# Performance work log

Measured on AMD Instinct MI355X. Metric: run time of the kernel, lower is better.

The kernel has to match this reference:

```python
import jax, jax.numpy as jnp
import numpy as np

N_NODES = 100000
N_EDGES = 1600000
FEATURE_DIM, CONDITION_DIM, HIDDEN_DIM, LATENT_DIM = 256, 64, 128, 64


def setup_inputs() -> dict:
    key = jax.random.key(0)
    ks = jax.random.split(key, 12)

    def glorot(k, fan_in, fan_out):
        s = np.sqrt(6.0 / (fan_in + fan_out)).astype(np.float32)
        return jax.random.uniform(k, (fan_in, fan_out), jnp.float32, -s, s)

    return {
        "feature": jax.random.normal(ks[0], (N_NODES, FEATURE_DIM), jnp.float32),
        "condition": jax.random.normal(ks[1], (N_NODES, CONDITION_DIM), jnp.float32),
        "edge_index": jax.random.randint(ks[2], (2, N_EDGES), 0, N_NODES, jnp.int64),
        "W_f2h": glorot(ks[3], FEATURE_DIM, HIDDEN_DIM),
        "b_f2h": jnp.zeros((HIDDEN_DIM,), jnp.float32),
        "W_c2h": glorot(ks[4], CONDITION_DIM, HIDDEN_DIM),
        "b_c2h": jnp.zeros((HIDDEN_DIM,), jnp.float32),
        "W_h2h": glorot(ks[5], 2 * HIDDEN_DIM, HIDDEN_DIM),
        "b_h2h": jnp.zeros((HIDDEN_DIM,), jnp.float32),
        "W_h2l": glorot(ks[6], HIDDEN_DIM, LATENT_DIM),
        "b_h2l": jnp.zeros((LATENT_DIM,), jnp.float32),
    }


def reference(feature, condition, edge_index, W_f2h, b_f2h, W_c2h, b_c2h,
              W_h2h, b_h2h, W_h2l, b_h2l):
    N = feature.shape[0]
    self_loops = jnp.arange(N, dtype=edge_index.dtype)
    src = jnp.concatenate([edge_index[0], self_loops])  # message sources (j)
    dst = jnp.concatenate([edge_index[1], self_loops])  # message targets (i)

    # symmetric GCN normalization: D^{-1/2} (A+I) D^{-1/2}
    deg = jax.ops.segment_sum(jnp.ones(dst.shape[0], feature.dtype), dst,
                              num_segments=N)
    dinv = jnp.where(deg > 0, jax.lax.rsqrt(deg), 0.0)
    norm = dinv[src] * dinv[dst]  # [E+N]

    def gcn_conv(x, W, b):
        xl = x @ W                                   # [N, out]
        msg = xl[src] * norm[:, None]                # gather + scale
        return jax.ops.segment_sum(msg, dst, num_segments=N) + b

    f2h = jnp.tanh(gcn_conv(feature, W_f2h, b_f2h))
    c2h = jnp.tanh(gcn_conv(condition, W_c2h, b_c2h))
    h = jnp.concatenate([f2h, c2h], axis=1)          # [N, 2*hidden]
    h = jnp.tanh(gcn_conv(h, W_h2h, b_h2h))
    z = gcn_conv(h, W_h2l, b_h2l)
    return z
```

## Files before the change

### kernel.cpp

```cpp
#include <hip/hip_runtime.h>
#include <cmath>
#include <cstdint>


typedef _Float16 f16;
typedef _Float16 f16x8 __attribute__((ext_vector_type(8)));
typedef _Float16 f16x4 __attribute__((ext_vector_type(4)));
typedef float f32x4 __attribute__((ext_vector_type(4)));
typedef unsigned int u32x4 __attribute__((ext_vector_type(4)));
typedef unsigned int u32x2 __attribute__((ext_vector_type(2)));

__global__ void count_zero_kernel(int* __restrict__ count, int N) {
    int i = blockIdx.x * 256 + threadIdx.x;
    if (i < N) count[i] = 0;
}

__global__ void count_rank_kernel(const int* __restrict__ dst, int* __restrict__ count,
                                  int* __restrict__ rank, int E) {
    int e = blockIdx.x * 256 + threadIdx.x;
    if (e < E) rank[e] = atomicAdd(&count[dst[e]], 1);
}

constexpr int SCAN_VPT = 8;
constexpr int SCAN_TILE = 256 * SCAN_VPT;

__global__ __launch_bounds__(256) void scan_partial_kernel(const int* __restrict__ count,
                                                           float* __restrict__ dinv,
                                                           int* __restrict__ blocksums, int N) {
    __shared__ int red[256];
    const int t = threadIdx.x;
    int base = blockIdx.x * SCAN_TILE + t * SCAN_VPT;
    int s = 0;
#pragma unroll
    for (int i = 0; i < SCAN_VPT; ++i) {
        int idx = base + i;
        if (idx < N) {
            int c = count[idx];
            dinv[idx] = rsqrtf((float)(c + 1));
            s += c;
        }
    }
    red[t] = s;
    __syncthreads();
    for (int off = 128; off > 0; off >>= 1) {
        if (t < off) red[t] += red[t + off];
        __syncthreads();
    }
    if (t == 0) blocksums[blockIdx.x] = red[0];
}

__global__ __launch_bounds__(256) void scan_final_kernel(const int* __restrict__ count,
                                                         const int* __restrict__ blocksums,
                                                         int* __restrict__ row_ptr, int N, int nb) {
    __shared__ int red[256];
    __shared__ int bs[64];
    const int t = threadIdx.x;
    if (t < 64) bs[t] = (t < nb) ? blocksums[t] : 0;
    __syncthreads();
    for (int off = 1; off < 64; off <<= 1) {
        int u = (t < 64 && t >= off) ? bs[t - off] : 0;
        __syncthreads();
        if (t < 64) bs[t] += u;
        __syncthreads();
    }
    const int myBase = (blockIdx.x > 0) ? bs[blockIdx.x - 1] : 0;

    int base = blockIdx.x * SCAN_TILE + t * SCAN_VPT;
    int vals[SCAN_VPT];
    int s = 0;
#pragma unroll
    for (int i = 0; i < SCAN_VPT; ++i) {
        int idx = base + i;
        vals[i] = (idx < N) ? count[idx] : 0;
        s += vals[i];
    }
    red[t] = s;
    __syncthreads();
    for (int off = 1; off < 256; off <<= 1) {
        int u = (t >= off) ? red[t - off] : 0;
        __syncthreads();
        red[t] += u;
        __syncthreads();
    }
    int run = red[t] - s + myBase;
#pragma unroll
    for (int i = 0; i < SCAN_VPT; ++i) {
        int idx = base + i;
        if (idx < N) {
            row_ptr[idx] = run;
            run += vals[i];
            if (idx == N - 1) row_ptr[N] = run;
        }
    }
}

__global__ void fill_kernel(const int* __restrict__ src, const int* __restrict__ dst,
                            const int* __restrict__ rank, const float* __restrict__ dinv,
                            const int* __restrict__ row_ptr, long long* __restrict__ csr, int E) {
    int e = blockIdx.x * 256 + threadIdx.x;
    if (e >= E) return;
    int s = src[e];
    int d = dst[e];
    int pos = row_ptr[d] + rank[e];
    float nrm = dinv[s] * dinv[d];
    long long v = ((long long)(unsigned)__float_as_int(nrm) << 32) | (unsigned)s;
    __builtin_nontemporal_store(v, csr + pos);
}

__device__ inline void wprep_one(const float* __restrict__ W, f16* __restrict__ hi,
                                 f16* __restrict__ lo, int M, int idx) {
    int k = idx / M, m = idx % M;
    float w = W[idx];
    f16 h = (f16)w;
    int f = ((k >> 5) * (M >> 4) + (m >> 4)) * 512 + (((k >> 3) & 3) << 7) + ((m & 15) << 3) + (k & 7);
    hi[f] = h;
    lo[f] = (f16)(w - (float)h);
}

__global__ void wprep_all_kernel(const float* __restrict__ W1, f16* h1, f16* l1,
                                 const float* __restrict__ W2, f16* h2, f16* l2,
                                 const float* __restrict__ W3, f16* h3, f16* l3,
                                 const float* __restrict__ W4, f16* h4, f16* l4) {
    int b = blockIdx.x;
    int t = threadIdx.x;
    if (b < 128) {
        wprep_one(W1, h1, l1, 128, b * 256 + t);
    } else if (b < 160) {
        wprep_one(W2, h2, l2, 128, (b - 128) * 256 + t);
    } else if (b < 288) {
        wprep_one(W3, h3, l3, 128, (b - 160) * 256 + t);
    } else {
        wprep_one(W4, h4, l4, 64, (b - 288) * 256 + t);
    }
}

__global__ void cond_to_xl_kernel(const float* __restrict__ x, f16* __restrict__ XL, int N) {
    int i = blockIdx.x * 256 + threadIdx.x;
    if (i >= N * 16) return;
    int node = i >> 4, q = i & 15;
    float4 v = ((const float4*)x)[i];
    union { f16 h[4]; uint2 u; } p;
    p.h[0] = (f16)v.x; p.h[1] = (f16)v.y; p.h[2] = (f16)v.z; p.h[3] = (f16)v.w;
    *(uint2*)(XL + (size_t)node * 192 + 128 + q * 4) = p.u;
}

template <int K, int M, bool BIAS_TANH, bool X_IS_HALF>
__global__ __launch_bounds__(256) void gemm_direct_kernel(
    const void* __restrict__ Xv, const f16* __restrict__ WFh,
    const f16* __restrict__ WFl, const float* __restrict__ bias,
    f16* __restrict__ out, int ld, int colOff, int ldx, int N) {
    constexpr int BM = 128;
    constexpr int SW = M / 4;
    constexpr int CT = SW / 16;
    constexpr int RT = BM / 16;
    constexpr int KS = K / 32;
    constexpr int MT = M / 16;

    const int tid = threadIdx.x;
    const int lane = tid & 63;
    const int wv = tid >> 6;
    const int m16 = lane & 15;
    const int quad = lane >> 4;
    const int row0 = blockIdx.x * BM;

    int xr[RT];
#pragma unroll
    for (int rt = 0; rt < RT; ++rt) {
        int r = row0 + rt * 16 + m16;
        xr[rt] = r < N ? r : N - 1;
    }

    f32x4 acc[RT][CT];
#pragma unroll
    for (int rt = 0; rt < RT; ++rt)
#pragma unroll
        for (int ct = 0; ct < CT; ++ct) acc[rt][ct] = (f32x4){0.f, 0.f, 0.f, 0.f};

    for (int ks = 0; ks < KS; ++ks) {
        const int k0 = ks * 32;
        f16x8 bh[CT], bl[CT];
#pragma unroll
        for (int ct = 0; ct < CT; ++ct) {
            const int fb = ((ks * MT + wv * CT + ct) << 9) + lane * 8;
            bh[ct] = *(const f16x8*)(WFh + fb);
            bl[ct] = *(const f16x8*)(WFl + fb);
        }
#pragma unroll
        for (int rt = 0; rt < RT; ++rt) {
            f16x8 a;
            if (X_IS_HALF) {
                a = *(const f16x8*)((const f16*)Xv + (size_t)xr[rt] * ldx + k0 + quad * 8);
            } else {
                const float* xp = (const float*)Xv + (size_t)xr[rt] * ldx + k0 + quad * 8;
                f32x4 v0 = *(const f32x4*)xp;
                f32x4 v1 = *(const f32x4*)(xp + 4);
                a[0] = (f16)v0[0]; a[1] = (f16)v0[1]; a[2] = (f16)v0[2]; a[3] = (f16)v0[3];
                a[4] = (f16)v1[0]; a[5] = (f16)v1[1]; a[6] = (f16)v1[2]; a[7] = (f16)v1[3];
            }
#pragma unroll
            for (int ct = 0; ct < CT; ++ct) {
                acc[rt][ct] = __builtin_amdgcn_mfma_f32_16x16x32_f16(a, bh[ct], acc[rt][ct], 0, 0, 0);
                acc[rt][ct] = __builtin_amdgcn_mfma_f32_16x16x32_f16(a, bl[ct], acc[rt][ct], 0, 0, 0);
            }
        }
    }

    float brs[CT];
    if (BIAS_TANH) {
#pragma unroll
        for (int ct = 0; ct < CT; ++ct) brs[ct] = bias[wv * SW + ct * 16 + m16];
    }

#pragma unroll
    for (int rt = 0; rt < RT; ++rt) {
#pragma unroll
        for (int r = 0; r < 4; ++r) {
            int row = row0 + rt * 16 + quad * 4 + r;
            if (row < N) {
                f16* op = out + (size_t)row * ld + colOff + wv * SW + m16;
#pragma unroll
                for (int ct = 0; ct < CT; ++ct) {
                    float v = acc[rt][ct][r];
                    if (BIAS_TANH) v = tanhf(v + brs[ct]);
                    op[ct * 16] = (f16)v;
                }
            }
        }
    }
}

template <int M, bool TANH, bool HAS_BIAS, bool OUT_F32>
__global__ __launch_bounds__(256) void gather_h_kernel(
    const f16* __restrict__ xl, const float* __restrict__ b,
    const float* __restrict__ dinv, const int* __restrict__ row_ptr,
    const long long* __restrict__ csr, void* __restrict__ outv,
    int ld, int colOff, int N) {
    constexpr int TPN = M / 8;
    int gid = blockIdx.x * 256 + threadIdx.x;
    int node = gid / TPN;
    int t = gid % TPN;
    if (node >= N) return;

    float di = dinv[node];
    float self = di * di;
    f16x8 x = *(const f16x8*)(xl + (size_t)node * M + t * 8);
    float acc[8];
#pragma unroll
    for (int j = 0; j < 8; ++j) acc[j] = (float)x[j] * self;
    if (HAS_BIAS) {
        float4 b0 = *(const float4*)(b + t * 8);
        float4 b1 = *(const float4*)(b + t * 8 + 4);
        acc[0] += b0.x; acc[1] += b0.y; acc[2] += b0.z; acc[3] += b0.w;
        acc[4] += b1.x; acc[5] += b1.y; acc[6] += b1.z; acc[7] += b1.w;
    }

    int p = row_ptr[node];
    const int p1 = row_ptr[node + 1];
    const int last = p1 - 1;
    long long e0 = 0, e1 = 0, e2 = 0, e3 = 0;
    if (p < p1) {
        e0 = __builtin_nontemporal_load(csr + p);
        e1 = __builtin_nontemporal_load(csr + (p + 1 < p1 ? p + 1 : last));
        e2 = __builtin_nontemporal_load(csr + (p + 2 < p1 ? p + 2 : last));
        e3 = __builtin_nontemporal_load(csr + (p + 3 < p1 ? p + 3 : last));
    }
    while (p < p1) {
        const long long c0 = e0, c1 = e1, c2 = e2, c3 = e3;
        const int pn = p + 4;
        if (pn < p1) {
            e0 = __builtin_nontemporal_load(csr + pn);
            e1 = __builtin_nontemporal_load(csr + (pn + 1 < p1 ? pn + 1 : last));
            e2 = __builtin_nontemporal_load(csr + (pn + 2 < p1 ? pn + 2 : last));
            e3 = __builtin_nontemporal_load(csr + (pn + 3 < p1 ? pn + 3 : last));
        }
        int s0 = (int)c0, s1 = (int)c1, s2 = (int)c2, s3 = (int)c3;
        float n0 = __int_as_float((int)(c0 >> 32));
        float n1 = (p + 1 < p1) ? __int_as_float((int)(c1 >> 32)) : 0.f;
        float n2 = (p + 2 < p1) ? __int_as_float((int)(c2 >> 32)) : 0.f;
        float n3 = (p + 3 < p1) ? __int_as_float((int)(c3 >> 32)) : 0.f;
        f16x8 v0 = *(const f16x8*)(xl + (size_t)s0 * M + t * 8);
        f16x8 v1 = *(const f16x8*)(xl + (size_t)s1 * M + t * 8);
        f16x8 v2 = *(const f16x8*)(xl + (size_t)s2 * M + t * 8);
        f16x8 v3 = *(const f16x8*)(xl + (size_t)s3 * M + t * 8);
#pragma unroll
        for (int j = 0; j < 8; ++j)
            acc[j] += ((float)v0[j] * n0 + (float)v1[j] * n1) +
                      ((float)v2[j] * n2 + (float)v3[j] * n3);
        p = pn;
    }

    if (TANH) {
#pragma unroll
        for (int j = 0; j < 8; ++j) acc[j] = tanhf(acc[j]);
    }

    if (OUT_F32) {
        float* op = (float*)outv + (size_t)node * ld + colOff + t * 8;
        f32x4 o0 = {acc[0], acc[1], acc[2], acc[3]};
        f32x4 o1 = {acc[4], acc[5], acc[6], acc[7]};
        __builtin_nontemporal_store(o0, (f32x4*)op);
        __builtin_nontemporal_store(o1, (f32x4*)(op + 4));
    } else {
        union { f16 h[8]; u32x4 u; } o;
#pragma unroll
        for (int j = 0; j < 8; ++j) o.h[j] = (f16)acc[j];
        __builtin_nontemporal_store(o.u, (u32x4*)((f16*)outv + (size_t)node * ld + colOff + t * 8));
    }
}

__global__ __launch_bounds__(256) void gather_fused_kernel(
    const f16* __restrict__ XL, const float* __restrict__ bA,
    const float* __restrict__ dinv, const int* __restrict__ row_ptr,
    const long long* __restrict__ csr, f16* __restrict__ out, int N) {
    int gid = blockIdx.x * 256 + threadIdx.x;
    int node = gid >> 4;
    int t = gid & 15;
    if (node >= N) return;

    float di = dinv[node];
    float self = di * di;
    const f16* base = XL + (size_t)node * 192;
    f16x8 xa = *(const f16x8*)(base + t * 8);
    f16x4 xc = *(const f16x4*)(base + 128 + t * 4);
    float accA[8], accC[4];
#pragma unroll
    for (int j = 0; j < 8; ++j) accA[j] = (float)xa[j] * self;
#pragma unroll
    for (int j = 0; j < 4; ++j) accC[j] = (float)xc[j] * self;
    {
        float4 b0 = *(const float4*)(bA + t * 8);
        float4 b1 = *(const float4*)(bA + t * 8 + 4);
        accA[0] += b0.x; accA[1] += b0.y; accA[2] += b0.z; accA[3] += b0.w;
        accA[4] += b1.x; accA[5] += b1.y; accA[6] += b1.z; accA[7] += b1.w;
    }

    int p = row_ptr[node];
    const int p1 = row_ptr[node + 1];
    const int last = p1 - 1;
    long long e0 = 0, e1 = 0, e2 = 0, e3 = 0;
    if (p < p1) {
        e0 = __builtin_nontemporal_load(csr + p);
        e1 = __builtin_nontemporal_load(csr + (p + 1 < p1 ? p + 1 : last));
        e2 = __builtin_nontemporal_load(csr + (p + 2 < p1 ? p + 2 : last));
        e3 = __builtin_nontemporal_load(csr + (p + 3 < p1 ? p + 3 : last));
    }
    while (p < p1) {
        const long long c0 = e0, c1 = e1, c2 = e2, c3 = e3;
        const int pn = p + 4;
        if (pn < p1) {
            e0 = __builtin_nontemporal_load(csr + pn);
            e1 = __builtin_nontemporal_load(csr + (pn + 1 < p1 ? pn + 1 : last));
            e2 = __builtin_nontemporal_load(csr + (pn + 2 < p1 ? pn + 2 : last));
            e3 = __builtin_nontemporal_load(csr + (pn + 3 < p1 ? pn + 3 : last));
        }
        int s0 = (int)c0, s1 = (int)c1, s2 = (int)c2, s3 = (int)c3;
        float n0 = __int_as_float((int)(c0 >> 32));
        float n1 = (p + 1 < p1) ? __int_as_float((int)(c1 >> 32)) : 0.f;
        float n2 = (p + 2 < p1) ? __int_as_float((int)(c2 >> 32)) : 0.f;
        float n3 = (p + 3 < p1) ? __int_as_float((int)(c3 >> 32)) : 0.f;
        const f16* r0 = XL + (size_t)s0 * 192;
        const f16* r1 = XL + (size_t)s1 * 192;
        const f16* r2 = XL + (size_t)s2 * 192;
        const f16* r3 = XL + (size_t)s3 * 192;
        f16x8 a0 = *(const f16x8*)(r0 + t * 8);
        f16x8 a1 = *(const f16x8*)(r1 + t * 8);
        f16x8 a2 = *(const f16x8*)(r2 + t * 8);
        f16x8 a3 = *(const f16x8*)(r3 + t * 8);
        f16x4 q0 = *(const f16x4*)(r0 + 128 + t * 4);
        f16x4 q1 = *(const f16x4*)(r1 + 128 + t * 4);
        f16x4 q2 = *(const f16x4*)(r2 + 128 + t * 4);
        f16x4 q3 = *(const f16x4*)(r3 + 128 + t * 4);
#pragma unroll
        for (int j = 0; j < 8; ++j)
            accA[j] += ((float)a0[j] * n0 + (float)a1[j] * n1) +
                       ((float)a2[j] * n2 + (float)a3[j] * n3);
#pragma unroll
        for (int j = 0; j < 4; ++j)
            accC[j] += ((float)q0[j] * n0 + (float)q1[j] * n1) +
                       ((float)q2[j] * n2 + (float)q3[j] * n3);
        p = pn;
    }

#pragma unroll
    for (int j = 0; j < 8; ++j) accA[j] = tanhf(accA[j]);

    union { f16 h[8]; u32x4 u; } oa;
#pragma unroll
    for (int j = 0; j < 8; ++j) oa.h[j] = (f16)accA[j];
    __builtin_nontemporal_store(oa.u, (u32x4*)(out + (size_t)node * 256 + t * 8));
    union { f16 h[4]; u32x2 u; } oc;
#pragma unroll
    for (int j = 0; j < 4; ++j) oc.h[j] = (f16)accC[j];
    __builtin_nontemporal_store(oc.u, (u32x2*)(out + (size_t)node * 256 + 128 + t * 4));
}

extern "C" void kernel_launch(void* const* d_in, const int* in_sizes, int n_in,
                              void* d_out, int out_size, void* d_ws, size_t ws_size,
                              hipStream_t stream) {
    const int FD = 256;

    const float* feature   = (const float*)d_in[0];
    const float* condition = (const float*)d_in[1];
    const int*   edge      = (const int*)d_in[2];
    const float* W_f2h = (const float*)d_in[3];
    const float* b_f2h = (const float*)d_in[4];
    const float* W_c2h = (const float*)d_in[5];
    const float* b_c2h = (const float*)d_in[6];
    const float* W_h2h = (const float*)d_in[7];
    const float* b_h2h = (const float*)d_in[8];
    const float* W_h2l = (const float*)d_in[9];
    const float* b_h2l = (const float*)d_in[10];
    float* out = (float*)d_out;

    const int N = in_sizes[0] / FD;
    const int E = in_sizes[2] / 2;
    const int* src = edge;
    const int* dst = edge + E;

    float* ws_f   = (float*)d_ws;
    float* dinv   = ws_f;
    int*   count  = (int*)(ws_f + N);
    int*   rowp   = count + N;
    int*   bsums  = rowp + N + 1;
    int*   rank   = bsums + 1024;
    long long* csr = (long long*)(((uintptr_t)(rank + E) + 15) & ~(uintptr_t)15);
    f16*   XL     = (f16*)(csr + E);
    f16*   B_h    = XL + (size_t)N * 192;
    f16*   wt1h   = B_h + (size_t)N * 256;
    f16*   wt1l   = wt1h + 128 * 256;
    f16*   wt2h   = wt1l + 128 * 256;
    f16*   wt2l   = wt2h + 128 * 64;
    f16*   wt3h   = wt2l + 128 * 64;
    f16*   wt3l   = wt3h + 128 * 256;
    f16*   wt4h   = wt3l + 128 * 256;
    f16*   wt4l   = wt4h + 64 * 128;

    const int TB = 256;
    dim3 blk(TB);
    const int nScanBlocks = (N + SCAN_TILE - 1) / SCAN_TILE;

    wprep_all_kernel<<<320, blk, 0, stream>>>(W_f2h, wt1h, wt1l, W_c2h, wt2h, wt2l,
                                              W_h2h, wt3h, wt3l, W_h2l, wt4h, wt4l);
    cond_to_xl_kernel<<<(N * 16 + TB - 1) / TB, blk, 0, stream>>>(condition, XL, N);

    count_zero_kernel<<<(N + TB - 1) / TB, blk, 0, stream>>>(count, N);
    count_rank_kernel<<<(E + TB - 1) / TB, blk, 0, stream>>>(dst, count, rank, E);
    scan_partial_kernel<<<nScanBlocks, blk, 0, stream>>>(count, dinv, bsums, N);
    scan_final_kernel<<<nScanBlocks, blk, 0, stream>>>(count, bsums, rowp, N, nScanBlocks);
    fill_kernel<<<(E + TB - 1) / TB, blk, 0, stream>>>(src, dst, rank, dinv, rowp, csr, E);

    const int gemm_grid = (N + 127) / 128;
    const int g128 = (N * 16 + TB - 1) / TB;
    const int g64  = (N * 8 + TB - 1) / TB;

    gemm_direct_kernel<256, 128, false, false><<<gemm_grid, blk, 0, stream>>>(
        feature, wt1h, wt1l, nullptr, XL, 192, 0, 256, N);

    gather_fused_kernel<<<g128, blk, 0, stream>>>(
        XL, b_f2h, dinv, rowp, csr, B_h, N);

    gemm_direct_kernel<64, 128, true, true><<<gemm_grid, blk, 0, stream>>>(
        (const void*)(B_h + 128), wt2h, wt2l, b_c2h, B_h, 256, 128, 256, N);

    gemm_direct_kernel<256, 128, false, true><<<gemm_grid, blk, 0, stream>>>(
        B_h, wt3h, wt3l, nullptr, XL, 128, 0, 256, N);
    gather_h_kernel<128, true, true, false><<<g128, blk, 0, stream>>>(
        XL, b_h2h, dinv, rowp, csr, B_h, 128, 0, N);

    gemm_direct_kernel<128, 64, false, true><<<gemm_grid, blk, 0, stream>>>(
        B_h, wt4h, wt4l, nullptr, XL, 64, 0, 128, N);
    gather_h_kernel<64, false, true, true><<<g64, blk, 0, stream>>>(
        XL, b_h2l, dinv, rowp, csr, out, 64, 0, N);
}
```

Baseline: 750.1 us.

## Fuse conv2 GEMM into conv3 GEMM and fold W_h2l GEMM into conv3 gather

Merges the condition-branch GEMM (with bias+tanh) and the h2h GEMM into one kernel that keeps the c2h tile in LDS instead of writing and rereading it. It also fuses the third aggregation with the final 128x64 projection, doing the small MFMA from an LDS tile of tanh'd rows, so the intermediate hidden layer is never written to global memory. Smaller launches are merged too: the count-zero kernel becomes a memset and the condition conversion is folded into the weight-prep kernel. The trade-off is extra LDS use and a block barrier in the gather kernel, which may reduce occupancy.

New measurement: 693.6 us. 7.5% less time.

```diff
diff --git a/kernel.cpp b/kernel.cpp
--- a/kernel.cpp
+++ b/kernel.cpp
@@ -9,11 +9,6 @@
 typedef float f32x4 __attribute__((ext_vector_type(4)));
 typedef unsigned int u32x4 __attribute__((ext_vector_type(4)));
 typedef unsigned int u32x2 __attribute__((ext_vector_type(2)));
-
-__global__ void count_zero_kernel(int* __restrict__ count, int N) {
-    int i = blockIdx.x * 256 + threadIdx.x;
-    if (i < N) count[i] = 0;
-}
 
 __global__ void count_rank_kernel(const int* __restrict__ dst, int* __restrict__ count,
                                   int* __restrict__ rank, int E) {
@@ -120,7 +115,8 @@
 __global__ void wprep_all_kernel(const float* __restrict__ W1, f16* h1, f16* l1,
                                  const float* __restrict__ W2, f16* h2, f16* l2,
                                  const float* __restrict__ W3, f16* h3, f16* l3,
-                                 const float* __restrict__ W4, f16* h4, f16* l4) {
+                                 const float* __restrict__ W4, f16* h4, f16* l4,
+                                 const float* __restrict__ cond, f16* __restrict__ XL, int N) {
     int b = blockIdx.x;
     int t = threadIdx.x;
     if (b < 128) {
@@ -129,26 +125,25 @@
         wprep_one(W2, h2, l2, 128, (b - 128) * 256 + t);
     } else if (b < 288) {
         wprep_one(W3, h3, l3, 128, (b - 160) * 256 + t);
+    } else if (b < 320) {
+        wprep_one(W4, h4, l4, 64, (b - 288) * 256 + t);
     } else {
-        wprep_one(W4, h4, l4, 64, (b - 288) * 256 + t);
-    }
-}
-
-__global__ void cond_to_xl_kernel(const float* __restrict__ x, f16* __restrict__ XL, int N) {
-    int i = blockIdx.x * 256 + threadIdx.x;
-    if (i >= N * 16) return;
-    int node = i >> 4, q = i & 15;
-    float4 v = ((const float4*)x)[i];
-    union { f16 h[4]; uint2 u; } p;
-    p.h[0] = (f16)v.x; p.h[1] = (f16)v.y; p.h[2] = (f16)v.z; p.h[3] = (f16)v.w;
-    *(uint2*)(XL + (size_t)node * 192 + 128 + q * 4) = p.u;
-}
-
-template <int K, int M, bool BIAS_TANH, bool X_IS_HALF>
+        int i = (b - 320) * 256 + t;
+        if (i < N * 16) {
+            int node = i >> 4, q = i & 15;
+            float4 v = ((const float4*)cond)[i];
+            union { f16 h[4]; uint2 u; } p;
+            p.h[0] = (f16)v.x; p.h[1] = (f16)v.y; p.h[2] = (f16)v.z; p.h[3] = (f16)v.w;
+            *(uint2*)(XL + (size_t)node * 192 + 128 + q * 4) = p.u;
+        }
+    }
+}
+
+template <int K, int M, bool X_IS_HALF>
 __global__ __launch_bounds__(256) void gemm_direct_kernel(
     const void* __restrict__ Xv, const f16* __restrict__ WFh,
-    const f16* __restrict__ WFl, const float* __restrict__ bias,
-    f16* __restrict__ out, int ld, int colOff, int ldx, int N) {
+    const f16* __restrict__ WFl, f16* __restrict__ out,
+    int ld, int colOff, int ldx, int N) {
     constexpr int BM = 128;
     constexpr int SW = M / 4;
     constexpr int CT = SW / 16;
@@ -205,12 +200,6 @@
         }
     }
 
-    float brs[CT];
-    if (BIAS_TANH) {
-#pragma unroll
-        for (int ct = 0; ct < CT; ++ct) brs[ct] = bias[wv * SW + ct * 16 + m16];
-    }
-
 #pragma unroll
     for (int rt = 0; rt < RT; ++rt) {
 #pragma unroll
@@ -219,14 +208,114 @@
             if (row < N) {
                 f16* op = out + (size_t)row * ld + colOff + wv * SW + m16;
 #pragma unroll
+                for (int ct = 0; ct < CT; ++ct) op[ct * 16] = (f16)acc[rt][ct][r];
+            }
+        }
+    }
+}
+
+__global__ __launch_bounds__(256) void gemm_conv23_kernel(
+    const f16* __restrict__ Bh, const f16* __restrict__ W2h, const f16* __restrict__ W2l,
+    const float* __restrict__ b2, const f16* __restrict__ W3h, const f16* __restrict__ W3l,
+    f16* __restrict__ outXL, int N) {
+    constexpr int RT = 8, CT = 2, LP = 136;
+    __shared__ f16 c2s[128 * LP];
+
+    const int tid = threadIdx.x;
+    const int lane = tid & 63;
+    const int wv = tid >> 6;
+    const int m16 = lane & 15;
+    const int quad = lane >> 4;
+    const int row0 = blockIdx.x * 128;
+
+    int xr[RT];
+#pragma unroll
+    for (int rt = 0; rt < RT; ++rt) {
+        int r = row0 + rt * 16 + m16;
+        xr[rt] = r < N ? r : N - 1;
+    }
+
+    {
+        f32x4 acc2[RT][CT];
+#pragma unroll
+        for (int rt = 0; rt < RT; ++rt)
+#pragma unroll
+            for (int ct = 0; ct < CT; ++ct) acc2[rt][ct] = (f32x4){0.f, 0.f, 0.f, 0.f};
+#pragma unroll
+        for (int ks = 0; ks < 2; ++ks) {
+            f16x8 bh[CT], bl[CT];
+#pragma unroll
+            for (int ct = 0; ct < CT; ++ct) {
+                const int fb = ((ks * 8 + wv * CT + ct) << 9) + lane * 8;
+                bh[ct] = *(const f16x8*)(W2h + fb);
+                bl[ct] = *(const f16x8*)(W2l + fb);
+            }
+#pragma unroll
+            for (int rt = 0; rt < RT; ++rt) {
+                f16x8 a = *(const f16x8*)(Bh + (size_t)xr[rt] * 256 + 128 + ks * 32 + quad * 8);
+#pragma unroll
                 for (int ct = 0; ct < CT; ++ct) {
-                    float v = acc[rt][ct][r];
-                    if (BIAS_TANH) v = tanhf(v + brs[ct]);
-                    op[ct * 16] = (f16)v;
+                    acc2[rt][ct] = __builtin_amdgcn_mfma_f32_16x16x32_f16(a, bh[ct], acc2[rt][ct], 0, 0, 0);
+                    acc2[rt][ct] = __builtin_amdgcn_mfma_f32_16x16x32_f16(a, bl[ct], acc2[rt][ct], 0, 0, 0);
                 }
             }
         }
-    }
+        float b2r[CT];
+#pragma unroll
+        for (int ct = 0; ct < CT; ++ct) b2r[ct] = b2[wv * 32 + ct * 16 + m16];
+#pragma unroll
+        for (int rt = 0; rt < RT; ++rt)
+#pragma unroll
+            for (int r = 0; r < 4; ++r) {
+                int row = rt * 16 + quad * 4 + r;
+#pragma unroll
+                for (int ct = 0; ct < CT; ++ct)
+                    c2s[row * LP + wv * 32 + ct * 16 + m16] = (f16)tanhf(acc2[rt][ct][r] + b2r[ct]);
+            }
+    }
+    __syncthreads();
+
+    f32x4 acc3[RT][CT];
+#pragma unroll
+    for (int rt = 0; rt < RT; ++rt)
+#pragma unroll
+        for (int ct = 0; ct < CT; ++ct) acc3[rt][ct] = (f32x4){0.f, 0.f, 0.f, 0.f};
+#pragma unroll
+    for (int ks = 0; ks < 8; ++ks) {
+        f16x8 bh[CT], bl[CT];
+#pragma unroll
+        for (int ct = 0; ct < CT; ++ct) {
+            const int fb = ((ks * 8 + wv * CT + ct) << 9) + lane * 8;
+            bh[ct] = *(const f16x8*)(W3h + fb);
+            bl[ct] = *(const f16x8*)(W3l + fb);
+        }
+#pragma unroll
+        for (int rt = 0; rt < RT; ++rt) {
+            f16x8 a;
+            if (ks < 4) {
+                a = *(const f16x8*)(Bh + (size_t)xr[rt] * 256 + ks * 32 + quad * 8);
+            } else {
+                a = *(const f16x8*)(&c2s[(rt * 16 + m16) * LP + (ks - 4) * 32 + quad * 8]);
+            }
+#pragma unroll
+            for (int ct = 0; ct < CT; ++ct) {
+                acc3[rt][ct] = __builtin_amdgcn_mfma_f32_16x16x32_f16(a, bh[ct], acc3[rt][ct], 0, 0, 0);
+                acc3[rt][ct] = __builtin_amdgcn_mfma_f32_16x16x32_f16(a, bl[ct], acc3[rt][ct], 0, 0, 0);
+            }
+        }
+    }
+
+#pragma unroll
+    for (int rt = 0; rt < RT; ++rt)
+#pragma unroll
+        for (int r = 0; r < 4; ++r) {
+            int row = row0 + rt * 16 + quad * 4 + r;
+            if (row < N) {
+                f16* op = outXL + (size_t)row * 128 + wv * 32 + m16;
+#pragma unroll
+                for (int ct = 0; ct < CT; ++ct) op[ct * 16] = (f16)acc3[rt][ct][r];
+            }
+        }
 }
 
 template <int M, bool TANH, bool HAS_BIAS, bool OUT_F32>
@@ -394,6 +483,97 @@
     __builtin_nontemporal_store(oc.u, (u32x2*)(out + (size_t)node * 256 + 128 + t * 4));
 }
 
+__global__ __launch_bounds__(256) void gather34_kernel(
+    const f16* __restrict__ xl, const float* __restrict__ b,
+    const float* __restrict__ dinv, const int* __restrict__ row_ptr,
+    const long long* __restrict__ csr, const f16* __restrict__ W4h,
+    const f16* __restrict__ W4l, f16* __restrict__ zpre, int N) {
+    constexpr int LP = 136;
+    __shared__ f16 h2s[16 * LP];
+    const int tid = threadIdx.x;
+    const int nloc = tid >> 4;
+    const int t = tid & 15;
+    const int node = blockIdx.x * 16 + nloc;
+    const bool active = node < N;
+
+    float acc[8];
+    if (active) {
+        float di = dinv[node];
+        float self = di * di;
+        f16x8 x = *(const f16x8*)(xl + (size_t)node * 128 + t * 8);
+#pragma unroll
+        for (int j = 0; j < 8; ++j) acc[j] = (float)x[j] * self;
+        {
+            float4 b0 = *(const float4*)(b + t * 8);
+            float4 b1 = *(const float4*)(b + t * 8 + 4);
+            acc[0] += b0.x; acc[1] += b0.y; acc[2] += b0.z; acc[3] += b0.w;
+            acc[4] += b1.x; acc[5] += b1.y; acc[6] += b1.z; acc[7] += b1.w;
+        }
+
+        int p = row_ptr[node];
+        const int p1 = row_ptr[node + 1];
+        const int last = p1 - 1;
+        long long e0 = 0, e1 = 0, e2 = 0, e3 = 0;
+        if (p < p1) {
+            e0 = __builtin_nontemporal_load(csr + p);
+            e1 = __builtin_nontemporal_load(csr + (p + 1 < p1 ? p + 1 : last));
+            e2 = __builtin_nontemporal_load(csr + (p + 2 < p1 ? p + 2 : last));
+            e3 = __builtin_nontemporal_load(csr + (p + 3 < p1 ? p + 3 : last));
+        }
+        while (p < p1) {
+            const long long c0 = e0, c1 = e1, c2 = e2, c3 = e3;
+            const int pn = p + 4;
+            if (pn < p1) {
+                e0 = __builtin_nontemporal_load(csr + pn);
+                e1 = __builtin_nontemporal_load(csr + (pn + 1 < p1 ? pn + 1 : last));
+                e2 = __builtin_nontemporal_load(csr + (pn + 2 < p1 ? pn + 2 : last));
+                e3 = __builtin_nontemporal_load(csr + (pn + 3 < p1 ? pn + 3 : last));
+            }
+            int s0 = (int)c0, s1 = (int)c1, s2 = (int)c2, s3 = (int)c3;
+            float n0 = __int_as_float((int)(c0 >> 32));
+            float n1 = (p + 1 < p1) ? __int_as_float((int)(c1 >> 32)) : 0.f;
+            float n2 = (p + 2 < p1) ? __int_as_float((int)(c2 >> 32)) : 0.f;
+            float n3 = (p + 3 < p1) ? __int_as_float((int)(c3 >> 32)) : 0.f;
+            f16x8 v0 = *(const f16x8*)(xl + (size_t)s0 * 128 + t * 8);
+            f16x8 v1 = *(const f16x8*)(xl + (size_t)s1 * 128 + t * 8);
+            f16x8 v2 = *(const f16x8*)(xl + (size_t)s2 * 128 + t * 8);
+            f16x8 v3 = *(const f16x8*)(xl + (size_t)s3 * 128 + t * 8);
+#pragma unroll
+            for (int j = 0; j < 8; ++j)
+                acc[j] += ((float)v0[j] * n0 + (float)v1[j] * n1) +
+                          ((float)v2[j] * n2 + (float)v3[j] * n3);
+            p = pn;
+        }
+
+        union { f16 h[8]; u32x4 u; } o;
+#pragma unroll
+        for (int j = 0; j < 8; ++j) o.h[j] = (f16)tanhf(acc[j]);
+        *(u32x4*)(&h2s[nloc * LP + t * 8]) = o.u;
+    }
+    __syncthreads();
+
+    const int lane = tid & 63;
+    const int wv = tid >> 6;
+    const int m16 = lane & 15;
+    const int quad = lane >> 4;
+
+    f32x4 a4 = (f32x4){0.f, 0.f, 0.f, 0.f};
+#pragma unroll
+    for (int ks = 0; ks < 4; ++ks) {
+        f16x8 av = *(const f16x8*)(&h2s[m16 * LP + ks * 32 + quad * 8]);
+        const int fb = ((ks * 4 + wv) << 9) + lane * 8;
+        f16x8 bh = *(const f16x8*)(W4h + fb);
+        f16x8 bl = *(const f16x8*)(W4l + fb);
+        a4 = __builtin_amdgcn_mfma_f32_16x16x32_f16(av, bh, a4, 0, 0, 0);
+        a4 = __builtin_amdgcn_mfma_f32_16x16x32_f16(av, bl, a4, 0, 0, 0);
+    }
+#pragma unroll
+    for (int r = 0; r < 4; ++r) {
+        int g = blockIdx.x * 16 + quad * 4 + r;
+        if (g < N) zpre[(size_t)g * 64 + wv * 16 + m16] = (f16)a4[r];
+    }
+}
+
 extern "C" void kernel_launch(void* const* d_in, const int* in_sizes, int n_in,
                               void* d_out, int out_size, void* d_ws, size_t ws_size,
                               hipStream_t stream) {
@@ -438,12 +618,13 @@
     const int TB = 256;
     dim3 blk(TB);
     const int nScanBlocks = (N + SCAN_TILE - 1) / SCAN_TILE;
-
-    wprep_all_kernel<<<320, blk, 0, stream>>>(W_f2h, wt1h, wt1l, W_c2h, wt2h, wt2l,
-                                              W_h2h, wt3h, wt3l, W_h2l, wt4h, wt4l);
-    cond_to_xl_kernel<<<(N * 16 + TB - 1) / TB, blk, 0, stream>>>(condition, XL, N);
-
-    count_zero_kernel<<<(N + TB - 1) / TB, blk, 0, stream>>>(count, N);
+    const int condBlocks = (N * 16 + TB - 1) / TB;
+
+    hipMemsetAsync(count, 0, (size_t)N * sizeof(int), stream);
+    wprep_all_kernel<<<320 + condBlocks, blk, 0, stream>>>(
+        W_f2h, wt1h, wt1l, W_c2h, wt2h, wt2l, W_h2h, wt3h, wt3l, W_h2l, wt4h, wt4l,
+        condition, XL, N);
+
     count_rank_kernel<<<(E + TB - 1) / TB, blk, 0, stream>>>(dst, count, rank, E);
     scan_partial_kernel<<<nScanBlocks, blk, 0, stream>>>(count, dinv, bsums, N);
     scan_final_kernel<<<nScanBlocks, blk, 0, stream>>>(count, bsums, rowp, N, nScanBlocks);
@@ -453,22 +634,18 @@
     const int g128 = (N * 16 + TB - 1) / TB;
     const int g64  = (N * 8 + TB - 1) / TB;
 
-    gemm_direct_kernel<256, 128, false, false><<<gemm_grid, blk, 0, stream>>>(
-        feature, wt1h, wt1l, nullptr, XL, 192, 0, 256, N);
+    gemm_direct_kernel<256, 128, false><<<gemm_grid, blk, 0, stream>>>(
+        feature, wt1h, wt1l, XL, 192, 0, 256, N);
 
     gather_fused_kernel<<<g128, blk, 0, stream>>>(
         XL, b_f2h, dinv, rowp, csr, B_h, N);
 
-    gemm_direct_kernel<64, 128, true, true><<<gemm_grid, blk, 0, stream>>>(
-        (const void*)(B_h + 128), wt2h, wt2l, b_c2h, B_h, 256, 128, 256, N);
-
-    gemm_direct_kernel<256, 128, false, true><<<gemm_grid, blk, 0, stream>>>(
-        B_h, wt3h, wt3l, nullptr, XL, 128, 0, 256, N);
-    gather_h_kernel<128, true, true, false><<<g128, blk, 0, stream>>>(
-        XL, b_h2h, dinv, rowp, csr, B_h, 128, 0, N);
-
-    gemm_direct_kernel<128, 64, false, true><<<gemm_grid, blk, 0, stream>>>(
-        B_h, wt4h, wt4l, nullptr, XL, 64, 0, 128, N);
+    gemm_conv23_kernel<<<gemm_grid, blk, 0, stream>>>(
+        B_h, wt2h, wt2l, b_c2h, wt3h, wt3l, XL, N);
+
+    gather34_kernel<<<g128, blk, 0, stream>>>(
+        XL, b_h2h, dinv, rowp, csr, wt4h, wt4l, B_h, N);
+
     gather_h_kernel<64, false, true, true><<<g64, blk, 0, stream>>>(
-        XL, b_h2l, dinv, rowp, csr, out, 64, 0, N);
-}
+        B_h, b_h2l, dinv, rowp, csr, out, 64, 0, N);
+}
```
